# Optimization experiments

Measured on AMD Instinct MI355X. Metric: run time of the kernel, lower is better.

Reference implementation:

```python
import jax, jax.numpy as jnp
import numpy as np

SIZES = [384, 160, 128, 96, 1]   # aev_length followed by hidden sizes (ANI-1 config)
N_SPECIES = 4                    # H, C, N, O
N_LAYERS = 4
CELU_ALPHA = 0.1
B, A = 128, 512                  # molecules, atoms per molecule


def setup_inputs() -> dict:
    key = jax.random.key(0)
    ks = jax.random.split(key, 2 + 2 * N_LAYERS)
    inp = {
        "fullaev": jax.random.normal(ks[0], (B, A, SIZES[0]), dtype=jnp.float32),
        "species": jax.random.randint(ks[1], (A,), 0, N_SPECIES, dtype=jnp.int32),
    }
    # Per-species stacked Linear params, torch default init: U(-1/sqrt(fan_in), 1/sqrt(fan_in))
    for l in range(N_LAYERS):
        bound = 1.0 / np.sqrt(SIZES[l])
        inp[f"W{l}"] = jax.random.uniform(ks[2 + 2 * l], (N_SPECIES, SIZES[l + 1], SIZES[l]),
                                          dtype=jnp.float32, minval=-bound, maxval=bound)
        inp[f"b{l}"] = jax.random.uniform(ks[3 + 2 * l], (N_SPECIES, SIZES[l + 1]),
                                          dtype=jnp.float32, minval=-bound, maxval=bound)
    return inp


def reference(fullaev, species, W0, b0, W1, b1, W2, b2, W3, b3):
    # fullaev: [B, A, aev_len]; species: [A] int route ids.
    # Equivalent to the per-atom Python loop: each atom goes through its
    # species' MLP; gather the per-atom weight matrices and do one batched GEMM per layer.
    Ws = (W0, W1, W2, W3)
    bs = (b0, b1, b2, b3)
    y = fullaev
    for l in range(N_LAYERS):
        Wa = Ws[l][species]          # [A, out, in] gathered per atom
        ba = bs[l][species]          # [A, out]
        y = jnp.einsum('bai,aoi->bao', y, Wa) + ba[None, :, :]
        if l < N_LAYERS - 1:
            y = jax.nn.celu(y, alpha=CELU_ALPHA)
    # stack over atoms + sum reducer over atom dim, then squeeze -> [B]
    return jnp.squeeze(jnp.sum(y, axis=1), axis=-1)
```

## Files before the change

### kernel.cpp

```cpp
#include <hip/hip_runtime.h>


typedef float f32x4 __attribute__((ext_vector_type(4)));
typedef short s16x8 __attribute__((ext_vector_type(8)));

#define NMOL   128
#define NATOM  512
#define AEV    384
#define MT     64
#define XLD    136
#define Y0LD   168
#define Y1LD   136
#define Y2LD   104

#define PL0    61440
#define PL1    20480
#define PL2    12288
#define BASE0  0
#define BASE1  245760
#define BASE2  327680
#define WP_BYTE_OFF 262144

__device__ __forceinline__ ushort f2bf(float f) {
    uint u = __float_as_uint(f);
    return (ushort)((u + 0x7fffu + ((u >> 16) & 1u)) >> 16);
}
__device__ __forceinline__ float bf2f(ushort h) {
    return __uint_as_float(((uint)h) << 16);
}
__device__ __forceinline__ float celu_f(float v) {
    return fmaxf(v, 0.0f) + fminf(0.1f * (__expf(10.0f * v) - 1.0f), 0.0f);
}

__global__ __launch_bounds__(256) void prep_kernel(
    const float* __restrict__ W0, const float* __restrict__ W1,
    const float* __restrict__ W2, ushort* __restrict__ Wp)
{
    const int idx = blockIdx.x * 256 + threadIdx.x;
    int n, k, KS;
    size_t base;
    float f;
    if (idx < 245760) {
        const int s = idx / PL0, r = idx % PL0;
        n = r / 384; k = r % 384; KS = 12;
        f = W0[idx];
        base = BASE0 + (size_t)s * PL0;
    } else if (idx < 327680) {
        const int i2 = idx - 245760;
        const int s = i2 / PL1, r = i2 % PL1;
        n = r / 160; k = r % 160; KS = 5;
        f = W1[i2];
        base = BASE1 + (size_t)s * PL1;
    } else {
        const int i2 = idx - 327680;
        const int s = i2 / PL2, r = i2 % PL2;
        n = r / 128; k = r % 128; KS = 4;
        f = W2[i2];
        base = BASE2 + (size_t)s * PL2;
    }
    const size_t fo = (size_t)((((n >> 4) * KS + (k >> 5)) * 64
                                + ((k & 31) >> 3) * 16 + (n & 15)) * 8 + (k & 7));
    Wp[base + fo] = f2bf(f);
}

__global__ __launch_bounds__(512, 4) void ani_mfma_kernel(
    const float* __restrict__ aev, const int* __restrict__ species,
    const ushort* __restrict__ Wp,
    const float* __restrict__ b0, const float* __restrict__ b1,
    const float* __restrict__ b2,
    const float* __restrict__ W3, const float* __restrict__ b3,
    float* __restrict__ partial)
{
    __shared__ __align__(16) ushort xbuf[2 * MT * XLD];
    __shared__ __align__(16) ushort ybuf[MT * Y0LD];

    const int bid  = blockIdx.x;
    const int a    = bid >> 1;
    const int half = bid & 1;
    const int tid  = threadIdx.x;
    const int lane = tid & 63;
    const int wid  = tid >> 6;
    const int mgrp = wid >> 2;
    const int ngrp = wid & 3;
    const bool has3 = (ngrp < 2);

    const int mol0 = tid >> 5;
    const int c4   = tid & 31;
    const float*  xp   = aev + ((size_t)(half * MT + mol0) * NATOM + a) * AEV + c4 * 4;
    const size_t  PSTR = (size_t)16 * NATOM * AEV;

    float4 rv[4];
    #pragma unroll
    for (int p = 0; p < 4; ++p) rv[p] = *(const float4*)(xp + p * PSTR);

    const int s = species[a];
    const ushort* Bh0 = Wp + BASE0 + (size_t)s * PL0;
    const ushort* Bh1 = Wp + BASE1 + (size_t)s * PL1;
    const ushort* Bh2 = Wp + BASE2 + (size_t)s * PL2;
    const float* b0s = b0 + s * 160;
    const float* b1s = b1 + s * 128;
    const float* b2s = b2 + s * 96;
    const float* w3s = W3 + s * 96;
    const float  bb3 = b3[s];

    ushort* X0 = xbuf;
    ushort* X1 = xbuf + MT * XLD;

    auto stage = [&](ushort* dst) {
        #pragma unroll
        for (int p = 0; p < 4; ++p) {
            uint2 ph;
            ph.x = (uint)f2bf(rv[p].x) | ((uint)f2bf(rv[p].y) << 16);
            ph.y = (uint)f2bf(rv[p].z) | ((uint)f2bf(rv[p].w) << 16);
            *(uint2*)(dst + (mol0 + 16 * p) * XLD + c4 * 4) = ph;
        }
    };

    s16x8 bl[3][4];
    auto l0_bload = [&](int tile) {
        #pragma unroll
        for (int ks = 0; ks < 4; ++ks) {
            const int gks = tile * 4 + ks;
            bl[0][ks] = *(const s16x8*)(Bh0 + ((size_t)((ngrp     ) * 12 + gks) * 64 + lane) * 8);
            bl[1][ks] = *(const s16x8*)(Bh0 + ((size_t)((ngrp +  4) * 12 + gks) * 64 + lane) * 8);
        }
        if (has3) {
            #pragma unroll
            for (int ks = 0; ks < 4; ++ks) {
                const int gks = tile * 4 + ks;
                bl[2][ks] = *(const s16x8*)(Bh0 + ((size_t)((ngrp + 8) * 12 + gks) * 64 + lane) * 8);
            }
        }
    };

    f32x4 acc[2][3];
    const f32x4 zero = {0.f, 0.f, 0.f, 0.f};
    #pragma unroll
    for (int mf = 0; mf < 2; ++mf)
        #pragma unroll
        for (int t = 0; t < 3; ++t) acc[mf][t] = zero;

    auto l0_tile = [&](const ushort* Xb) {
        #pragma unroll
        for (int ks = 0; ks < 4; ++ks) {
            s16x8 ah[2];
            #pragma unroll
            for (int mf = 0; mf < 2; ++mf)
                ah[mf] = *(const s16x8*)(Xb + (mgrp * 32 + mf * 16 + (lane & 15)) * XLD
                                         + ks * 32 + (lane >> 4) * 8);
            #pragma unroll
            for (int mf = 0; mf < 2; ++mf) {
                acc[mf][0] = __builtin_amdgcn_mfma_f32_16x16x32_bf16(ah[mf], bl[0][ks], acc[mf][0], 0, 0, 0);
                acc[mf][1] = __builtin_amdgcn_mfma_f32_16x16x32_bf16(ah[mf], bl[1][ks], acc[mf][1], 0, 0, 0);
            }
            if (has3) {
                #pragma unroll
                for (int mf = 0; mf < 2; ++mf)
                    acc[mf][2] = __builtin_amdgcn_mfma_f32_16x16x32_bf16(ah[mf], bl[2][ks], acc[mf][2], 0, 0, 0);
            }
        }
    };

    stage(X0);
    l0_bload(0);
    #pragma unroll
    for (int p = 0; p < 4; ++p) rv[p] = *(const float4*)(xp + 128 + p * PSTR);
    __syncthreads();

    l0_tile(X0);
    l0_bload(1);
    stage(X1);
    #pragma unroll
    for (int p = 0; p < 4; ++p) rv[p] = *(const float4*)(xp + 256 + p * PSTR);
    __syncthreads();

    l0_tile(X1);
    l0_bload(2);
    stage(X0);
    __syncthreads();

    l0_tile(X0);

    s16x8 b1r[2][5];
    #pragma unroll
    for (int ks = 0; ks < 5; ++ks) {
        b1r[0][ks] = *(const s16x8*)(Bh1 + ((size_t)((ngrp    ) * 5 + ks) * 64 + lane) * 8);
        b1r[1][ks] = *(const s16x8*)(Bh1 + ((size_t)((ngrp + 4) * 5 + ks) * 64 + lane) * 8);
    }

    #pragma unroll
    for (int t = 0; t < 3; ++t) {
        if (t < 2 || has3) {
            const int n = (ngrp + 4 * t) * 16 + (lane & 15);
            const float bv = b0s[n];
            #pragma unroll
            for (int mf = 0; mf < 2; ++mf) {
                #pragma unroll
                for (int r = 0; r < 4; ++r) {
                    const int row = mgrp * 32 + mf * 16 + (lane >> 4) * 4 + r;
                    ybuf[row * Y0LD + n] = f2bf(celu_f(acc[mf][t][r] + bv));
                }
            }
        }
    }
    __syncthreads();

    f32x4 acc1[2][2];
    #pragma unroll
    for (int mf = 0; mf < 2; ++mf) { acc1[mf][0] = zero; acc1[mf][1] = zero; }
    #pragma unroll
    for (int ks = 0; ks < 5; ++ks) {
        s16x8 ah[2];
        #pragma unroll
        for (int mf = 0; mf < 2; ++mf)
            ah[mf] = *(const s16x8*)(ybuf + (mgrp * 32 + mf * 16 + (lane & 15)) * Y0LD
                                     + ks * 32 + (lane >> 4) * 8);
        #pragma unroll
        for (int mf = 0; mf < 2; ++mf) {
            acc1[mf][0] = __builtin_amdgcn_mfma_f32_16x16x32_bf16(ah[mf], b1r[0][ks], acc1[mf][0], 0, 0, 0);
            acc1[mf][1] = __builtin_amdgcn_mfma_f32_16x16x32_bf16(ah[mf], b1r[1][ks], acc1[mf][1], 0, 0, 0);
        }
    }

    s16x8 b2r[2][4];
    #pragma unroll
    for (int ks = 0; ks < 4; ++ks)
        b2r[0][ks] = *(const s16x8*)(Bh2 + ((size_t)((ngrp) * 4 + ks) * 64 + lane) * 8);
    if (has3) {
        #pragma unroll
        for (int ks = 0; ks < 4; ++ks)
            b2r[1][ks] = *(const s16x8*)(Bh2 + ((size_t)((ngrp + 4) * 4 + ks) * 64 + lane) * 8);
    }

    ushort* Y1h = xbuf;
    #pragma unroll
    for (int t = 0; t < 2; ++t) {
        const int n = (ngrp + 4 * t) * 16 + (lane & 15);
        const float bv = b1s[n];
        #pragma unroll
        for (int mf = 0; mf < 2; ++mf) {
            #pragma unroll
            for (int r = 0; r < 4; ++r) {
                const int row = mgrp * 32 + mf * 16 + (lane >> 4) * 4 + r;
                Y1h[row * Y1LD + n] = f2bf(celu_f(acc1[mf][t][r] + bv));
            }
        }
    }
    __syncthreads();

    f32x4 acc2[2][2];
    #pragma unroll
    for (int mf = 0; mf < 2; ++mf) { acc2[mf][0] = zero; acc2[mf][1] = zero; }
    #pragma unroll
    for (int ks = 0; ks < 4; ++ks) {
        s16x8 ah[2];
        #pragma unroll
        for (int mf = 0; mf < 2; ++mf)
            ah[mf] = *(const s16x8*)(Y1h + (mgrp * 32 + mf * 16 + (lane & 15)) * Y1LD
                                     + ks * 32 + (lane >> 4) * 8);
        #pragma unroll
        for (int mf = 0; mf < 2; ++mf) {
            acc2[mf][0] = __builtin_amdgcn_mfma_f32_16x16x32_bf16(ah[mf], b2r[0][ks], acc2[mf][0], 0, 0, 0);
            if (has3)
                acc2[mf][1] = __builtin_amdgcn_mfma_f32_16x16x32_bf16(ah[mf], b2r[1][ks], acc2[mf][1], 0, 0, 0);
        }
    }

    ushort* Y2h = ybuf;
    #pragma unroll
    for (int t = 0; t < 2; ++t) {
        if (t == 0 || has3) {
            const int n = (ngrp + 4 * t) * 16 + (lane & 15);
            const float bv = b2s[n];
            #pragma unroll
            for (int mf = 0; mf < 2; ++mf) {
                #pragma unroll
                for (int r = 0; r < 4; ++r) {
                    const int row = mgrp * 32 + mf * 16 + (lane >> 4) * 4 + r;
                    Y2h[row * Y2LD + n] = f2bf(celu_f(acc2[mf][t][r] + bv));
                }
            }
        }
    }
    __syncthreads();

    {
        float* red = (float*)xbuf;
        const int m = tid & (MT - 1);
        const int q = tid >> 6;
        float accv = 0.f;
        #pragma unroll
        for (int ii = 0; ii < 12; ++ii) {
            const int i = q * 12 + ii;
            accv = fmaf(w3s[i], bf2f(Y2h[m * Y2LD + i]), accv);
        }
        red[q * MT + m] = accv;
        __syncthreads();
        if (tid < MT) {
            float sm = bb3;
            #pragma unroll
            for (int qq = 0; qq < 8; ++qq) sm += red[qq * MT + tid];
            partial[(size_t)a * NMOL + half * MT + tid] = sm;
        }
    }
}

__global__ __launch_bounds__(256) void reduce_kernel(
    const float* __restrict__ partial, float* __restrict__ out)
{
    __shared__ float red[256];
    const int m = blockIdx.x;
    const int t = threadIdx.x;
    float sv = partial[(size_t)t * NMOL + m] + partial[(size_t)(t + 256) * NMOL + m];
    red[t] = sv;
    __syncthreads();
    #pragma unroll
    for (int w = 128; w > 0; w >>= 1) {
        if (t < w) red[t] += red[t + w];
        __syncthreads();
    }
    if (t == 0) out[m] = red[0];
}

extern "C" void kernel_launch(void* const* d_in, const int* in_sizes, int n_in,
                              void* d_out, int out_size, void* d_ws, size_t ws_size,
                              hipStream_t stream) {
    const float* aev     = (const float*)d_in[0];
    const int*   species = (const int*)  d_in[1];
    const float* W0 = (const float*)d_in[2];
    const float* b0 = (const float*)d_in[3];
    const float* W1 = (const float*)d_in[4];
    const float* b1 = (const float*)d_in[5];
    const float* W2 = (const float*)d_in[6];
    const float* b2 = (const float*)d_in[7];
    const float* W3 = (const float*)d_in[8];
    const float* b3 = (const float*)d_in[9];
    float* out     = (float*)d_out;
    float* partial = (float*)d_ws;
    ushort* Wp     = (ushort*)((char*)d_ws + WP_BYTE_OFF);

    prep_kernel<<<1472, 256, 0, stream>>>(W0, W1, W2, Wp);
    ani_mfma_kernel<<<NATOM * 2, 512, 0, stream>>>(aev, species, Wp,
                                                   b0, b1, b2, W3, b3, partial);
    reduce_kernel<<<NMOL, 256, 0, stream>>>(partial, out);
}
```

Baseline: 43.05 us.

## Process two atoms per block with cross-atom prefetch; vectorize weight prep

The main kernel now runs half as many blocks, each handling two atoms (a and a+256) in a loop. While layers 1–3 of the first atom run, it prefetches the second atom's AEV rows, stages them to LDS, and loads its layer-0 weight fragments, overlapping global latency with compute. To allow this, separate LDS buffers are used for the layer-0 and layer-1 activations. The prep kernel converts eight weights per thread with float4 loads and uint4 stores, so it launches far fewer threads. The trade-offs are larger LDS use per block, which may lower occupancy, and halving the grid, which leaves fewer blocks to spread across the CUs.

Measured after the change: 75.74 us. 75.9% more time.

```diff
diff --git a/kernel.cpp b/kernel.cpp
--- a/kernel.cpp
+++ b/kernel.cpp
@@ -37,30 +37,37 @@
     const float* __restrict__ W2, ushort* __restrict__ Wp)
 {
     const int idx = blockIdx.x * 256 + threadIdx.x;
-    int n, k, KS;
+    int n, k0, KS;
     size_t base;
-    float f;
-    if (idx < 245760) {
-        const int s = idx / PL0, r = idx % PL0;
-        n = r / 384; k = r % 384; KS = 12;
-        f = W0[idx];
+    const float* src;
+    if (idx < 30720) {
+        const int s = idx / 7680, r = idx % 7680;
+        n = r / 48; k0 = (r % 48) * 8; KS = 12;
+        src = W0 + (size_t)idx * 8;
         base = BASE0 + (size_t)s * PL0;
-    } else if (idx < 327680) {
-        const int i2 = idx - 245760;
-        const int s = i2 / PL1, r = i2 % PL1;
-        n = r / 160; k = r % 160; KS = 5;
-        f = W1[i2];
+    } else if (idx < 40960) {
+        const int i2 = idx - 30720;
+        const int s = i2 / 2560, r = i2 % 2560;
+        n = r / 20; k0 = (r % 20) * 8; KS = 5;
+        src = W1 + (size_t)i2 * 8;
         base = BASE1 + (size_t)s * PL1;
     } else {
-        const int i2 = idx - 327680;
-        const int s = i2 / PL2, r = i2 % PL2;
-        n = r / 128; k = r % 128; KS = 4;
-        f = W2[i2];
+        const int i2 = idx - 40960;
+        const int s = i2 / 1536, r = i2 % 1536;
+        n = r / 16; k0 = (r % 16) * 8; KS = 4;
+        src = W2 + (size_t)i2 * 8;
         base = BASE2 + (size_t)s * PL2;
     }
-    const size_t fo = (size_t)((((n >> 4) * KS + (k >> 5)) * 64
-                                + ((k & 31) >> 3) * 16 + (n & 15)) * 8 + (k & 7));
-    Wp[base + fo] = f2bf(f);
+    const float4 v0 = *(const float4*)(src);
+    const float4 v1 = *(const float4*)(src + 4);
+    const size_t fo = (size_t)((((n >> 4) * KS + (k0 >> 5)) * 64
+                                + ((k0 & 31) >> 3) * 16 + (n & 15)) * 8);
+    uint4 w;
+    w.x = (uint)f2bf(v0.x) | ((uint)f2bf(v0.y) << 16);
+    w.y = (uint)f2bf(v0.z) | ((uint)f2bf(v0.w) << 16);
+    w.z = (uint)f2bf(v1.x) | ((uint)f2bf(v1.y) << 16);
+    w.w = (uint)f2bf(v1.z) | ((uint)f2bf(v1.w) << 16);
+    *(uint4*)(Wp + base + fo) = w;
 }
 
 __global__ __launch_bounds__(512, 4) void ani_mfma_kernel(
@@ -72,10 +79,11 @@
     float* __restrict__ partial)
 {
     __shared__ __align__(16) ushort xbuf[2 * MT * XLD];
-    __shared__ __align__(16) ushort ybuf[MT * Y0LD];
+    __shared__ __align__(16) ushort y0buf[MT * Y0LD];
+    __shared__ __align__(16) ushort y1buf[MT * Y1LD];
 
     const int bid  = blockIdx.x;
-    const int a    = bid >> 1;
+    int a          = bid >> 1;
     const int half = bid & 1;
     const int tid  = threadIdx.x;
     const int lane = tid & 63;
@@ -86,14 +94,10 @@
 
     const int mol0 = tid >> 5;
     const int c4   = tid & 31;
-    const float*  xp   = aev + ((size_t)(half * MT + mol0) * NATOM + a) * AEV + c4 * 4;
-    const size_t  PSTR = (size_t)16 * NATOM * AEV;
-
-    float4 rv[4];
-    #pragma unroll
-    for (int p = 0; p < 4; ++p) rv[p] = *(const float4*)(xp + p * PSTR);
-
-    const int s = species[a];
+    const size_t PSTR = (size_t)16 * NATOM * AEV;
+    const float* xp = aev + ((size_t)(half * MT + mol0) * NATOM + a) * AEV + c4 * 4;
+
+    int s = species[a];
     const ushort* Bh0 = Wp + BASE0 + (size_t)s * PL0;
     const ushort* Bh1 = Wp + BASE1 + (size_t)s * PL1;
     const ushort* Bh2 = Wp + BASE2 + (size_t)s * PL2;
@@ -101,11 +105,17 @@
     const float* b1s = b1 + s * 128;
     const float* b2s = b2 + s * 96;
     const float* w3s = W3 + s * 96;
-    const float  bb3 = b3[s];
+    float        bb3 = b3[s];
 
     ushort* X0 = xbuf;
     ushort* X1 = xbuf + MT * XLD;
 
+    float4 rv[4];
+    auto prefetch_rv = [&](int t) {
+        #pragma unroll
+        for (int p = 0; p < 4; ++p)
+            rv[p] = *(const float4*)(xp + t * 128 + p * PSTR);
+    };
     auto stage = [&](ushort* dst) {
         #pragma unroll
         for (int p = 0; p < 4; ++p) {
@@ -121,8 +131,8 @@
         #pragma unroll
         for (int ks = 0; ks < 4; ++ks) {
             const int gks = tile * 4 + ks;
-            bl[0][ks] = *(const s16x8*)(Bh0 + ((size_t)((ngrp     ) * 12 + gks) * 64 + lane) * 8);
-            bl[1][ks] = *(const s16x8*)(Bh0 + ((size_t)((ngrp +  4) * 12 + gks) * 64 + lane) * 8);
+            bl[0][ks] = *(const s16x8*)(Bh0 + ((size_t)((ngrp    ) * 12 + gks) * 64 + lane) * 8);
+            bl[1][ks] = *(const s16x8*)(Bh0 + ((size_t)((ngrp + 4) * 12 + gks) * 64 + lane) * 8);
         }
         if (has3) {
             #pragma unroll
@@ -135,10 +145,6 @@
 
     f32x4 acc[2][3];
     const f32x4 zero = {0.f, 0.f, 0.f, 0.f};
-    #pragma unroll
-    for (int mf = 0; mf < 2; ++mf)
-        #pragma unroll
-        for (int t = 0; t < 3; ++t) acc[mf][t] = zero;
 
     auto l0_tile = [&](const ushort* Xb) {
         #pragma unroll
@@ -161,146 +167,173 @@
         }
     };
 
+    prefetch_rv(0);
     stage(X0);
     l0_bload(0);
-    #pragma unroll
-    for (int p = 0; p < 4; ++p) rv[p] = *(const float4*)(xp + 128 + p * PSTR);
+    prefetch_rv(1);
     __syncthreads();
 
-    l0_tile(X0);
-    l0_bload(1);
-    stage(X1);
-    #pragma unroll
-    for (int p = 0; p < 4; ++p) rv[p] = *(const float4*)(xp + 256 + p * PSTR);
-    __syncthreads();
-
-    l0_tile(X1);
-    l0_bload(2);
-    stage(X0);
-    __syncthreads();
-
-    l0_tile(X0);
-
-    s16x8 b1r[2][5];
-    #pragma unroll
-    for (int ks = 0; ks < 5; ++ks) {
-        b1r[0][ks] = *(const s16x8*)(Bh1 + ((size_t)((ngrp    ) * 5 + ks) * 64 + lane) * 8);
-        b1r[1][ks] = *(const s16x8*)(Bh1 + ((size_t)((ngrp + 4) * 5 + ks) * 64 + lane) * 8);
-    }
-
-    #pragma unroll
-    for (int t = 0; t < 3; ++t) {
-        if (t < 2 || has3) {
+    for (int ui = 0; ui < 2; ++ui) {
+        const bool more = (ui == 0);
+
+        #pragma unroll
+        for (int mf = 0; mf < 2; ++mf)
+            #pragma unroll
+            for (int t = 0; t < 3; ++t) acc[mf][t] = zero;
+
+        l0_tile(X0);  l0_bload(1);  stage(X1);  prefetch_rv(2);
+        __syncthreads();
+        l0_tile(X1);  l0_bload(2);  stage(X0);
+        __syncthreads();
+        l0_tile(X0);
+
+        s16x8 b1r[2][5];
+        #pragma unroll
+        for (int ks = 0; ks < 5; ++ks) {
+            b1r[0][ks] = *(const s16x8*)(Bh1 + ((size_t)((ngrp    ) * 5 + ks) * 64 + lane) * 8);
+            b1r[1][ks] = *(const s16x8*)(Bh1 + ((size_t)((ngrp + 4) * 5 + ks) * 64 + lane) * 8);
+        }
+
+        #pragma unroll
+        for (int t = 0; t < 3; ++t) {
+            if (t < 2 || has3) {
+                const int n = (ngrp + 4 * t) * 16 + (lane & 15);
+                const float bv = b0s[n];
+                #pragma unroll
+                for (int mf = 0; mf < 2; ++mf) {
+                    #pragma unroll
+                    for (int r = 0; r < 4; ++r) {
+                        const int row = mgrp * 32 + mf * 16 + (lane >> 4) * 4 + r;
+                        y0buf[row * Y0LD + n] = f2bf(celu_f(acc[mf][t][r] + bv));
+                    }
+                }
+            }
+        }
+        __syncthreads();
+
+        int s2 = 0;
+        if (more) {
+            s2 = species[a + 256];
+            xp += 256 * AEV;
+            prefetch_rv(0);
+        }
+
+        f32x4 acc1[2][2];
+        #pragma unroll
+        for (int mf = 0; mf < 2; ++mf) { acc1[mf][0] = zero; acc1[mf][1] = zero; }
+        #pragma unroll
+        for (int ks = 0; ks < 5; ++ks) {
+            s16x8 ah[2];
+            #pragma unroll
+            for (int mf = 0; mf < 2; ++mf)
+                ah[mf] = *(const s16x8*)(y0buf + (mgrp * 32 + mf * 16 + (lane & 15)) * Y0LD
+                                         + ks * 32 + (lane >> 4) * 8);
+            #pragma unroll
+            for (int mf = 0; mf < 2; ++mf) {
+                acc1[mf][0] = __builtin_amdgcn_mfma_f32_16x16x32_bf16(ah[mf], b1r[0][ks], acc1[mf][0], 0, 0, 0);
+                acc1[mf][1] = __builtin_amdgcn_mfma_f32_16x16x32_bf16(ah[mf], b1r[1][ks], acc1[mf][1], 0, 0, 0);
+            }
+        }
+
+        s16x8 b2r[2][4];
+        #pragma unroll
+        for (int ks = 0; ks < 4; ++ks)
+            b2r[0][ks] = *(const s16x8*)(Bh2 + ((size_t)((ngrp) * 4 + ks) * 64 + lane) * 8);
+        if (has3) {
+            #pragma unroll
+            for (int ks = 0; ks < 4; ++ks)
+                b2r[1][ks] = *(const s16x8*)(Bh2 + ((size_t)((ngrp + 4) * 4 + ks) * 64 + lane) * 8);
+        }
+
+        #pragma unroll
+        for (int t = 0; t < 2; ++t) {
             const int n = (ngrp + 4 * t) * 16 + (lane & 15);
-            const float bv = b0s[n];
+            const float bv = b1s[n];
             #pragma unroll
             for (int mf = 0; mf < 2; ++mf) {
                 #pragma unroll
                 for (int r = 0; r < 4; ++r) {
                     const int row = mgrp * 32 + mf * 16 + (lane >> 4) * 4 + r;
-                    ybuf[row * Y0LD + n] = f2bf(celu_f(acc[mf][t][r] + bv));
+                    y1buf[row * Y1LD + n] = f2bf(celu_f(acc1[mf][t][r] + bv));
                 }
             }
         }
-    }
-    __syncthreads();
-
-    f32x4 acc1[2][2];
-    #pragma unroll
-    for (int mf = 0; mf < 2; ++mf) { acc1[mf][0] = zero; acc1[mf][1] = zero; }
-    #pragma unroll
-    for (int ks = 0; ks < 5; ++ks) {
-        s16x8 ah[2];
-        #pragma unroll
-        for (int mf = 0; mf < 2; ++mf)
-            ah[mf] = *(const s16x8*)(ybuf + (mgrp * 32 + mf * 16 + (lane & 15)) * Y0LD
-                                     + ks * 32 + (lane >> 4) * 8);
-        #pragma unroll
-        for (int mf = 0; mf < 2; ++mf) {
-            acc1[mf][0] = __builtin_amdgcn_mfma_f32_16x16x32_bf16(ah[mf], b1r[0][ks], acc1[mf][0], 0, 0, 0);
-            acc1[mf][1] = __builtin_amdgcn_mfma_f32_16x16x32_bf16(ah[mf], b1r[1][ks], acc1[mf][1], 0, 0, 0);
-        }
-    }
-
-    s16x8 b2r[2][4];
-    #pragma unroll
-    for (int ks = 0; ks < 4; ++ks)
-        b2r[0][ks] = *(const s16x8*)(Bh2 + ((size_t)((ngrp) * 4 + ks) * 64 + lane) * 8);
-    if (has3) {
-        #pragma unroll
-        for (int ks = 0; ks < 4; ++ks)
-            b2r[1][ks] = *(const s16x8*)(Bh2 + ((size_t)((ngrp + 4) * 4 + ks) * 64 + lane) * 8);
-    }
-
-    ushort* Y1h = xbuf;
-    #pragma unroll
-    for (int t = 0; t < 2; ++t) {
-        const int n = (ngrp + 4 * t) * 16 + (lane & 15);
-        const float bv = b1s[n];
-        #pragma unroll
-        for (int mf = 0; mf < 2; ++mf) {
-            #pragma unroll
-            for (int r = 0; r < 4; ++r) {
-                const int row = mgrp * 32 + mf * 16 + (lane >> 4) * 4 + r;
-                Y1h[row * Y1LD + n] = f2bf(celu_f(acc1[mf][t][r] + bv));
-            }
-        }
-    }
-    __syncthreads();
-
-    f32x4 acc2[2][2];
-    #pragma unroll
-    for (int mf = 0; mf < 2; ++mf) { acc2[mf][0] = zero; acc2[mf][1] = zero; }
-    #pragma unroll
-    for (int ks = 0; ks < 4; ++ks) {
-        s16x8 ah[2];
-        #pragma unroll
-        for (int mf = 0; mf < 2; ++mf)
-            ah[mf] = *(const s16x8*)(Y1h + (mgrp * 32 + mf * 16 + (lane & 15)) * Y1LD
-                                     + ks * 32 + (lane >> 4) * 8);
-        #pragma unroll
-        for (int mf = 0; mf < 2; ++mf) {
-            acc2[mf][0] = __builtin_amdgcn_mfma_f32_16x16x32_bf16(ah[mf], b2r[0][ks], acc2[mf][0], 0, 0, 0);
-            if (has3)
-                acc2[mf][1] = __builtin_amdgcn_mfma_f32_16x16x32_bf16(ah[mf], b2r[1][ks], acc2[mf][1], 0, 0, 0);
-        }
-    }
-
-    ushort* Y2h = ybuf;
-    #pragma unroll
-    for (int t = 0; t < 2; ++t) {
-        if (t == 0 || has3) {
-            const int n = (ngrp + 4 * t) * 16 + (lane & 15);
-            const float bv = b2s[n];
+        __syncthreads();
+
+        if (more) {
+            stage(X0);
+            prefetch_rv(1);
+        }
+
+        f32x4 acc2[2][2];
+        #pragma unroll
+        for (int mf = 0; mf < 2; ++mf) { acc2[mf][0] = zero; acc2[mf][1] = zero; }
+        #pragma unroll
+        for (int ks = 0; ks < 4; ++ks) {
+            s16x8 ah[2];
+            #pragma unroll
+            for (int mf = 0; mf < 2; ++mf)
+                ah[mf] = *(const s16x8*)(y1buf + (mgrp * 32 + mf * 16 + (lane & 15)) * Y1LD
+                                         + ks * 32 + (lane >> 4) * 8);
             #pragma unroll
             for (int mf = 0; mf < 2; ++mf) {
-                #pragma unroll
-                for (int r = 0; r < 4; ++r) {
-                    const int row = mgrp * 32 + mf * 16 + (lane >> 4) * 4 + r;
-                    Y2h[row * Y2LD + n] = f2bf(celu_f(acc2[mf][t][r] + bv));
+                acc2[mf][0] = __builtin_amdgcn_mfma_f32_16x16x32_bf16(ah[mf], b2r[0][ks], acc2[mf][0], 0, 0, 0);
+                if (has3)
+                    acc2[mf][1] = __builtin_amdgcn_mfma_f32_16x16x32_bf16(ah[mf], b2r[1][ks], acc2[mf][1], 0, 0, 0);
+            }
+        }
+
+        #pragma unroll
+        for (int t = 0; t < 2; ++t) {
+            if (t == 0 || has3) {
+                const int n = (ngrp + 4 * t) * 16 + (lane & 15);
+                const float bv = b2s[n];
+                #pragma unroll
+                for (int mf = 0; mf < 2; ++mf) {
+                    #pragma unroll
+                    for (int r = 0; r < 4; ++r) {
+                        const int row = mgrp * 32 + mf * 16 + (lane >> 4) * 4 + r;
+                        y0buf[row * Y2LD + n] = f2bf(celu_f(acc2[mf][t][r] + bv));
+                    }
                 }
             }
         }
-    }
-    __syncthreads();
-
-    {
-        float* red = (float*)xbuf;
-        const int m = tid & (MT - 1);
-        const int q = tid >> 6;
-        float accv = 0.f;
-        #pragma unroll
-        for (int ii = 0; ii < 12; ++ii) {
-            const int i = q * 12 + ii;
-            accv = fmaf(w3s[i], bf2f(Y2h[m * Y2LD + i]), accv);
-        }
-        red[q * MT + m] = accv;
-        __syncthreads();
-        if (tid < MT) {
-            float sm = bb3;
-            #pragma unroll
-            for (int qq = 0; qq < 8; ++qq) sm += red[qq * MT + tid];
-            partial[(size_t)a * NMOL + half * MT + tid] = sm;
+        __syncthreads();
+
+        if (more) {
+            Bh0 = Wp + BASE0 + (size_t)s2 * PL0;
+            l0_bload(0);
+        }
+
+        {
+            float* red = (float*)y1buf;
+            const int m = tid & (MT - 1);
+            const int q = tid >> 6;
+            float accv = 0.f;
+            #pragma unroll
+            for (int ii = 0; ii < 12; ++ii) {
+                const int i = q * 12 + ii;
+                accv = fmaf(w3s[i], bf2f(y0buf[m * Y2LD + i]), accv);
+            }
+            red[q * MT + m] = accv;
+            __syncthreads();
+            if (tid < MT) {
+                float sm = bb3;
+                #pragma unroll
+                for (int qq = 0; qq < 8; ++qq) sm += red[qq * MT + tid];
+                partial[(size_t)a * NMOL + half * MT + tid] = sm;
+            }
+        }
+
+        if (more) {
+            Bh1 = Wp + BASE1 + (size_t)s2 * PL1;
+            Bh2 = Wp + BASE2 + (size_t)s2 * PL2;
+            b0s = b0 + s2 * 160;
+            b1s = b1 + s2 * 128;
+            b2s = b2 + s2 * 96;
+            w3s = W3 + s2 * 96;
+            bb3 = b3[s2];
+            a += 256;
         }
     }
 }
@@ -339,8 +372,8 @@
     float* partial = (float*)d_ws;
     ushort* Wp     = (ushort*)((char*)d_ws + WP_BYTE_OFF);
 
-    prep_kernel<<<1472, 256, 0, stream>>>(W0, W1, W2, Wp);
-    ani_mfma_kernel<<<NATOM * 2, 512, 0, stream>>>(aev, species, Wp,
-                                                   b0, b1, b2, W3, b3, partial);
+    prep_kernel<<<184, 256, 0, stream>>>(W0, W1, W2, Wp);
+    ani_mfma_kernel<<<512, 512, 0, stream>>>(aev, species, Wp,
+                                             b0, b1, b2, W3, b3, partial);
     reduce_kernel<<<NMOL, 256, 0, stream>>>(partial, out);
 }
```
